# Optimization experiments

Hardware: AMD Instinct MI355X
Metric: run time of the kernel (lower is better)

The kernel has to match this reference:

```python
import jax, jax.numpy as jnp
import numpy as np

NUM_NODES = 16384   # batch_size * nodes_per_query_graph
NODES_PER_GRAPH = 8
NUM_EDGES = 14336   # ~7 edges per query graph
NUM_RELS = 64
DIM = 128
BATCH = NUM_NODES // NODES_PER_GRAPH  # 2048
NUM_PASSES = 2
EPS = 1e-8


def setup_inputs() -> dict:
    key = jax.random.key(0)
    ks = jax.random.split(key, 7)
    x = jax.random.normal(ks[0], (NUM_NODES, DIM), jnp.float32)
    basis = jax.random.normal(ks[1], (NUM_RELS, DIM, DIM), jnp.float32) * 0.05
    root = jax.random.normal(ks[2], (DIM, DIM), jnp.float32) * 0.05
    bias = jax.random.normal(ks[3], (DIM,), jnp.float32) * 0.05
    target_embeds = jax.random.normal(ks[4], (BATCH, DIM), jnp.float32)
    # edges stay within each query graph: pick local src/dst per graph
    graph_of_edge = jnp.repeat(jnp.arange(BATCH), NUM_EDGES // BATCH)
    local = jax.random.randint(ks[5], (2, NUM_EDGES), 0, NODES_PER_GRAPH)
    edge_index = graph_of_edge[None, :] * NODES_PER_GRAPH + local  # [2, E]
    edge_type = jax.random.randint(ks[6], (NUM_EDGES,), 0, NUM_RELS)
    batch_idx = jnp.arange(NUM_NODES) // NODES_PER_GRAPH  # node -> query graph id
    return {"x": x, "basis": basis, "root": root, "bias": bias,
            "target_embeds": target_embeds, "edge_index": edge_index,
            "edge_type": edge_type, "batch_idx": batch_idx}


def rgcn_conv(h, edge_index, edge_type, basis, root, bias):
    # RGCNConv forward (num_bases=0, 'add' aggregation, no edge_norm)
    src, dst = edge_index[0], edge_index[1]
    w = basis[edge_type]                      # [E, D, D] relation-indexed gather
    msg = jnp.einsum('ed,edo->eo', h[src], w)  # per-edge bmm
    aggr = jax.ops.segment_sum(msg, dst, num_segments=h.shape[0])  # scatter-add
    return aggr + h @ root + bias


def reference(x, basis, root, bias, target_embeds, edge_index, edge_type, batch_idx):
    h = x
    for _ in range(NUM_PASSES - 1):
        h = jax.nn.relu(rgcn_conv(h, edge_index, edge_type, basis, root, bias))
    # sum readout per query graph (dropout=0 -> h2 == h1)
    pooled = jax.ops.segment_sum(h, batch_idx, num_segments=target_embeds.shape[0])
    # F.cosine_similarity(out, target_embeds, dim=1)
    num = jnp.sum(pooled * target_embeds, axis=1)
    na = jnp.maximum(jnp.linalg.norm(pooled, axis=1), EPS)
    nb = jnp.maximum(jnp.linalg.norm(target_embeds, axis=1), EPS)
    return num / (na * nb)
```

## Files before the change

kernel.cpp:

```cpp
#include <hip/hip_runtime.h>

#define NUM_NODES 16384
#define NPG 8
#define NUM_EDGES 14336
#define EPG 7
#define NUM_RELS 64
#define DIM 128
#define BATCH 2048
#define EPS 1e-8f

#define SEG 1792
#define ROOT_BLOCKS 256
#define EDGE_BLOCKS 512

using f16x8 = __attribute__((ext_vector_type(8))) _Float16;
using f32x4 = __attribute__((ext_vector_type(4))) float;

#define MSG_OFF 0u
#define RTP_OFF 3670016u
#define WS_NEEDED 7864320u

__global__ __launch_bounds__(256) void gemm2_kernel(
    const float* __restrict__ x, const float* __restrict__ basis,
    const float* __restrict__ root, const int* __restrict__ edge_index,
    const int* __restrict__ edge_type,
    _Float16* __restrict__ msg_h, _Float16* __restrict__ rootp_h)
{
    __shared__ _Float16 Bl[DIM * DIM];
    __shared__ int smeta[128];
    __shared__ int lcnt;

    const int bid = blockIdx.x;
    const int tid = threadIdx.x;
    const int lane = tid & 63;
    const int w    = tid >> 6;
    const bool isEdge = bid >= ROOT_BLOCKS;

    const float* Bsrc;

    if (isEdge) {
        if (tid < 64) { smeta[tid] = 0; smeta[64 + tid] = -1; }
        if (tid == 0) lcnt = 0;
        Bsrc = basis + ((size_t)((bid - ROOT_BLOCKS) >> 3) << 14);
    } else {
        const int row0 = bid * 64;
        if (tid < 64) {
            smeta[tid] = row0 + tid;
            smeta[64 + tid] = row0 + tid;
        }
        Bsrc = root;
    }
    __syncthreads();

    if (isEdge) {
        const int eb   = bid - ROOT_BLOCKS;
        const int rel  = eb >> 3;
        const int seg0 = (eb & 7) * SEG;
        #pragma unroll
        for (int it = 0; it < 7; ++it) {
            const int e = seg0 + it * 256 + tid;
            if (edge_type[e] == rel) {
                const int pos = atomicAdd(&lcnt, 1);
                if (pos < 64) {
                    smeta[pos] = edge_index[e];
                    smeta[64 + pos] = e;
                }
            }
        }
    }

    {
        const int br = tid >> 4;
        const int bc = tid & 15;
        const float* src = Bsrc + (br * 8) * DIM + bc * 8;
        _Float16 m[8][8];
        #pragma unroll
        for (int u = 0; u < 8; ++u) {
            const float4 a = *(const float4*)(src + u * DIM);
            const float4 b = *(const float4*)(src + u * DIM + 4);
            m[u][0] = (_Float16)a.x; m[u][1] = (_Float16)a.y;
            m[u][2] = (_Float16)a.z; m[u][3] = (_Float16)a.w;
            m[u][4] = (_Float16)b.x; m[u][5] = (_Float16)b.y;
            m[u][6] = (_Float16)b.z; m[u][7] = (_Float16)b.w;
        }
        #pragma unroll
        for (int c2 = 0; c2 < 8; ++c2) {
            const int col = bc * 8 + c2;
            const int chunk = col * 16 + br;
            const int cs = chunk ^ (c2 & 7) ^ (bc & 7);
            f16x8 v = {m[0][c2], m[1][c2], m[2][c2], m[3][c2],
                       m[4][c2], m[5][c2], m[6][c2], m[7][c2]};
            *(f16x8*)(&Bl[cs * 8]) = v;
        }
    }
    __syncthreads();

    if (isEdge && lcnt == 0) return;

    const int l15 = lane & 15;
    const int q   = lane >> 4;

    const int src = smeta[w * 16 + l15];
    const float* xrow = x + ((size_t)src << 7) + q * 8;
    f16x8 a[4];
    #pragma unroll
    for (int kb = 0; kb < 4; ++kb) {
        const float4 lo = *(const float4*)(xrow + kb * 32);
        const float4 hi = *(const float4*)(xrow + kb * 32 + 4);
        f16x8 av;
        av[0] = (_Float16)lo.x; av[1] = (_Float16)lo.y;
        av[2] = (_Float16)lo.z; av[3] = (_Float16)lo.w;
        av[4] = (_Float16)hi.x; av[5] = (_Float16)hi.y;
        av[6] = (_Float16)hi.z; av[7] = (_Float16)hi.w;
        a[kb] = av;
    }

    f32x4 acc[8];
    #pragma unroll
    for (int ct = 0; ct < 8; ++ct) acc[ct] = (f32x4){0.f, 0.f, 0.f, 0.f};

    #pragma unroll
    for (int ct = 0; ct < 8; ++ct) {
        const int col = ct * 16 + l15;
        const int sw  = (col & 7) ^ ((col >> 3) & 7);
        #pragma unroll
        for (int kb = 0; kb < 4; ++kb) {
            const int chunk = col * 16 + kb * 4 + q;
            const int cs = chunk ^ sw;
            const f16x8 bfr = *(const f16x8*)(&Bl[cs * 8]);
            acc[ct] = __builtin_amdgcn_mfma_f32_16x16x32_f16(a[kb], bfr, acc[ct], 0, 0, 0);
        }
    }

    _Float16* outb = isEdge ? msg_h : rootp_h;
    #pragma unroll
    for (int j = 0; j < 4; ++j) {
        const int r = w * 16 + q * 4 + j;
        const int oid = smeta[64 + r];
        if (oid >= 0) {
            #pragma unroll
            for (int ct = 0; ct < 8; ++ct) {
                outb[((size_t)oid << 7) + ct * 16 + l15] = (_Float16)acc[ct][j];
            }
        }
    }
}

__global__ __launch_bounds__(512) void finalize_kernel(
    const _Float16* __restrict__ rootp_h, const _Float16* __restrict__ msg_h,
    const float* __restrict__ bias, const float* __restrict__ target,
    const int* __restrict__ edge_index, float* __restrict__ out)
{
    const int g = blockIdx.x * 8 + (threadIdx.x >> 6);
    const int l = threadIdx.x & 63;
    const int d0 = l * 2;

    const float2 bv = *(const float2*)(bias + d0);
    float accA[NPG], accB[NPG];
    #pragma unroll
    for (int n = 0; n < NPG; ++n) {
        const _Float16* row = rootp_h + ((size_t)(g * NPG + n) << 7) + d0;
        accA[n] = bv.x + (float)row[0];
        accB[n] = bv.y + (float)row[1];
    }

    const int ebase = g * EPG;
    #pragma unroll
    for (int e = 0; e < EPG; ++e) {
        const int ge  = ebase + e;
        const int dst = edge_index[NUM_EDGES + ge] - g * NPG;
        const _Float16* mrow = msg_h + ((size_t)ge << 7) + d0;
        const float m0 = (float)mrow[0];
        const float m1 = (float)mrow[1];
        #pragma unroll
        for (int n = 0; n < NPG; ++n) {
            accA[n] += (n == dst) ? m0 : 0.f;
            accB[n] += (n == dst) ? m1 : 0.f;
        }
    }

    float p0 = 0.f, p1 = 0.f;
    #pragma unroll
    for (int n = 0; n < NPG; ++n) {
        p0 += fmaxf(accA[n], 0.f);
        p1 += fmaxf(accB[n], 0.f);
    }

    const float2 tv = *(const float2*)(target + (size_t)g * DIM + d0);
    float num_p = p0 * tv.x + p1 * tv.y;
    float na_p  = p0 * p0 + p1 * p1;
    float nb_p  = tv.x * tv.x + tv.y * tv.y;

    #pragma unroll
    for (int off = 32; off > 0; off >>= 1) {
        num_p += __shfl_down(num_p, off);
        na_p  += __shfl_down(na_p, off);
        nb_p  += __shfl_down(nb_p, off);
    }
    if (l == 0) {
        const float na = fmaxf(sqrtf(na_p), EPS);
        const float nb = fmaxf(sqrtf(nb_p), EPS);
        out[g] = num_p / (na * nb);
    }
}

__global__ __launch_bounds__(128) void rgcn_fused_kernel(
    const float* __restrict__ x, const float* __restrict__ basis,
    const float* __restrict__ root, const float* __restrict__ bias,
    const float* __restrict__ target, const int* __restrict__ edge_index,
    const int* __restrict__ edge_type, float* __restrict__ out)
{
    const int g = blockIdx.x;
    const int o = threadIdx.x;
    __shared__ float xs[NPG][DIM];
    __shared__ float red[6];
    {
        const float4* xg = reinterpret_cast<const float4*>(x + (size_t)g * NPG * DIM);
        float4* xs4 = reinterpret_cast<float4*>(&xs[0][0]);
        xs4[o] = xg[o];
        xs4[o + 128] = xg[o + 128];
    }
    __syncthreads();
    float acc[NPG];
    const float b = bias[o];
    #pragma unroll
    for (int n = 0; n < NPG; ++n) acc[n] = b;
    for (int d4 = 0; d4 < DIM / 4; ++d4) {
        const float r0 = root[(d4 * 4 + 0) * DIM + o];
        const float r1 = root[(d4 * 4 + 1) * DIM + o];
        const float r2 = root[(d4 * 4 + 2) * DIM + o];
        const float r3 = root[(d4 * 4 + 3) * DIM + o];
        #pragma unroll
        for (int n = 0; n < NPG; ++n) {
            const float4 xv = reinterpret_cast<const float4*>(&xs[n][0])[d4];
            acc[n] += xv.x * r0 + xv.y * r1 + xv.z * r2 + xv.w * r3;
        }
    }
    const int ebase = g * EPG;
    for (int e = 0; e < EPG; ++e) {
        const int ge  = ebase + e;
        const int src = edge_index[ge] - g * NPG;
        const int dst = edge_index[NUM_EDGES + ge] - g * NPG;
        const int rel = edge_type[ge];
        const float* __restrict__ B = basis + (size_t)rel * DIM * DIM;
        float m = 0.f;
        for (int d4 = 0; d4 < DIM / 4; ++d4) {
            const float4 xv = reinterpret_cast<const float4*>(&xs[src][0])[d4];
            m += xv.x * B[(d4 * 4 + 0) * DIM + o];
            m += xv.y * B[(d4 * 4 + 1) * DIM + o];
            m += xv.z * B[(d4 * 4 + 2) * DIM + o];
            m += xv.w * B[(d4 * 4 + 3) * DIM + o];
        }
        #pragma unroll
        for (int n = 0; n < NPG; ++n) acc[n] += (n == dst) ? m : 0.f;
    }
    float p = 0.f;
    #pragma unroll
    for (int n = 0; n < NPG; ++n) p += fmaxf(acc[n], 0.f);
    const float t = target[(size_t)g * DIM + o];
    float num_p = p * t, na_p = p * p, nb_p = t * t;
    #pragma unroll
    for (int off = 32; off > 0; off >>= 1) {
        num_p += __shfl_down(num_p, off);
        na_p  += __shfl_down(na_p, off);
        nb_p  += __shfl_down(nb_p, off);
    }
    const int wave = o >> 6, lane = o & 63;
    if (lane == 0) {
        red[wave * 3 + 0] = num_p;
        red[wave * 3 + 1] = na_p;
        red[wave * 3 + 2] = nb_p;
    }
    __syncthreads();
    if (o == 0) {
        const float num = red[0] + red[3];
        const float na  = fmaxf(sqrtf(red[1] + red[4]), EPS);
        const float nb  = fmaxf(sqrtf(red[2] + red[5]), EPS);
        out[g] = num / (na * nb);
    }
}

extern "C" void kernel_launch(void* const* d_in, const int* in_sizes, int n_in,
                              void* d_out, int out_size, void* d_ws, size_t ws_size,
                              hipStream_t stream) {
    const float* x          = (const float*)d_in[0];
    const float* basis      = (const float*)d_in[1];
    const float* root       = (const float*)d_in[2];
    const float* bias       = (const float*)d_in[3];
    const float* target     = (const float*)d_in[4];
    const int*   edge_index = (const int*)d_in[5];
    const int*   edge_type  = (const int*)d_in[6];
    float* out = (float*)d_out;

    if (ws_size < WS_NEEDED) {
        rgcn_fused_kernel<<<BATCH, 128, 0, stream>>>(
            x, basis, root, bias, target, edge_index, edge_type, out);
        return;
    }

    char* ws = (char*)d_ws;
    _Float16* msg_h   = (_Float16*)(ws + MSG_OFF);
    _Float16* rootp_h = (_Float16*)(ws + RTP_OFF);

    gemm2_kernel<<<ROOT_BLOCKS + EDGE_BLOCKS, 256, 0, stream>>>(
        x, basis, root, edge_index, edge_type, msg_h, rootp_h);
    finalize_kernel<<<BATCH / 8, 512, 0, stream>>>(
        rootp_h, msg_h, bias, target, edge_index, out);
}
```

Baseline: 22.25 us.

## Fuse finalize into GEMM kernel using per-edge ready flags and spin-waits

Merges the two launches into one kernel. Edge blocks are reordered to run first, and each publishes per-edge READY flags after a release fence. Root blocks keep their root-projection tile in LDS, spin on the flags for their 56 edges, then do the per-graph aggregation, ReLU, pooling and cosine similarity in place. This removes a kernel launch and the global round trip of the root projection. In exchange it relies on edge blocks being scheduled before or alongside the root blocks, and spin-waiting risks stalls or deadlock if they are not.

```diff
diff --git a/kernel.cpp b/kernel.cpp
--- a/kernel.cpp
+++ b/kernel.cpp
@@ -10,21 +10,25 @@
 #define EPS 1e-8f
 
 #define SEG 1792
+#define EDGE_BLOCKS 512
 #define ROOT_BLOCKS 256
-#define EDGE_BLOCKS 512
-
+#define READY 0x5A5A5A5A
+
+using f16x2 = __attribute__((ext_vector_type(2))) _Float16;
 using f16x8 = __attribute__((ext_vector_type(8))) _Float16;
 using f32x4 = __attribute__((ext_vector_type(4))) float;
 
-#define MSG_OFF 0u
-#define RTP_OFF 3670016u
-#define WS_NEEDED 7864320u
-
-__global__ __launch_bounds__(256) void gemm2_kernel(
+#define FLG_OFF 0u
+#define MSG_OFF 57344u
+#define DUM_OFF 3727360u
+#define WS_NEEDED 3727616u
+
+__global__ __launch_bounds__(256, 4) void rgcn_one_kernel(
     const float* __restrict__ x, const float* __restrict__ basis,
-    const float* __restrict__ root, const int* __restrict__ edge_index,
-    const int* __restrict__ edge_type,
-    _Float16* __restrict__ msg_h, _Float16* __restrict__ rootp_h)
+    const float* __restrict__ root, const float* __restrict__ bias,
+    const float* __restrict__ target, const int* __restrict__ edge_index,
+    const int* __restrict__ edge_type, float* __restrict__ out,
+    int* __restrict__ flags, _Float16* __restrict__ msg_h, int* __restrict__ dummy)
 {
     __shared__ _Float16 Bl[DIM * DIM];
     __shared__ int smeta[128];
@@ -34,16 +38,16 @@
     const int tid = threadIdx.x;
     const int lane = tid & 63;
     const int w    = tid >> 6;
-    const bool isEdge = bid >= ROOT_BLOCKS;
+    const bool isEdge = bid < EDGE_BLOCKS;
 
     const float* Bsrc;
 
     if (isEdge) {
         if (tid < 64) { smeta[tid] = 0; smeta[64 + tid] = -1; }
         if (tid == 0) lcnt = 0;
-        Bsrc = basis + ((size_t)((bid - ROOT_BLOCKS) >> 3) << 14);
+        Bsrc = basis + ((size_t)(bid >> 3) << 14);
     } else {
-        const int row0 = bid * 64;
+        const int row0 = (bid - EDGE_BLOCKS) * 64;
         if (tid < 64) {
             smeta[tid] = row0 + tid;
             smeta[64 + tid] = row0 + tid;
@@ -53,9 +57,8 @@
     __syncthreads();
 
     if (isEdge) {
-        const int eb   = bid - ROOT_BLOCKS;
-        const int rel  = eb >> 3;
-        const int seg0 = (eb & 7) * SEG;
+        const int rel  = bid >> 3;
+        const int seg0 = (bid & 7) * SEG;
         #pragma unroll
         for (int it = 0; it < 7; ++it) {
             const int e = seg0 + it * 256 + tid;
@@ -85,8 +88,7 @@
         }
         #pragma unroll
         for (int c2 = 0; c2 < 8; ++c2) {
-            const int col = bc * 8 + c2;
-            const int chunk = col * 16 + br;
+            const int chunk = (bc * 8 + c2) * 16 + br;
             const int cs = chunk ^ (c2 & 7) ^ (bc & 7);
             f16x8 v = {m[0][c2], m[1][c2], m[2][c2], m[3][c2],
                        m[4][c2], m[5][c2], m[6][c2], m[7][c2]};
@@ -100,8 +102,8 @@
     const int l15 = lane & 15;
     const int q   = lane >> 4;
 
-    const int src = smeta[w * 16 + l15];
-    const float* xrow = x + ((size_t)src << 7) + q * 8;
+    const int srcn = smeta[w * 16 + l15];
+    const float* xrow = x + ((size_t)srcn << 7) + q * 8;
     f16x8 a[4];
     #pragma unroll
     for (int kb = 0; kb < 4; ++kb) {
@@ -126,81 +128,111 @@
         #pragma unroll
         for (int kb = 0; kb < 4; ++kb) {
             const int chunk = col * 16 + kb * 4 + q;
-            const int cs = chunk ^ sw;
-            const f16x8 bfr = *(const f16x8*)(&Bl[cs * 8]);
+            const f16x8 bfr = *(const f16x8*)(&Bl[(chunk ^ sw) * 8]);
             acc[ct] = __builtin_amdgcn_mfma_f32_16x16x32_f16(a[kb], bfr, acc[ct], 0, 0, 0);
         }
     }
 
-    _Float16* outb = isEdge ? msg_h : rootp_h;
+    if (isEdge) {
+        #pragma unroll
+        for (int j = 0; j < 4; ++j) {
+            const int r = w * 16 + q * 4 + j;
+            const int oid = smeta[64 + r];
+            if (oid >= 0) {
+                #pragma unroll
+                for (int ct = 0; ct < 8; ++ct)
+                    msg_h[((size_t)oid << 7) + ct * 16 + l15] = (_Float16)acc[ct][j];
+            }
+        }
+        __syncthreads();
+        if (tid == 0)
+            __hip_atomic_fetch_add(dummy, 1, __ATOMIC_RELEASE, __HIP_MEMORY_SCOPE_AGENT);
+        __syncthreads();
+        if (tid < 64) {
+            const int oid = smeta[64 + tid];
+            if (oid >= 0)
+                (void)__hip_atomic_exchange(flags + oid, READY,
+                                            __ATOMIC_RELAXED, __HIP_MEMORY_SCOPE_AGENT);
+        }
+        return;
+    }
+
+    __syncthreads();
+    _Float16* Cl = Bl;
     #pragma unroll
     for (int j = 0; j < 4; ++j) {
-        const int r = w * 16 + q * 4 + j;
-        const int oid = smeta[64 + r];
-        if (oid >= 0) {
+        const int lr = w * 16 + q * 4 + j;
+        #pragma unroll
+        for (int ct = 0; ct < 8; ++ct)
+            Cl[lr * 132 + ct * 16 + l15] = (_Float16)acc[ct][j];
+    }
+    __syncthreads();
+
+    const int rb = bid - EDGE_BLOCKS;
+    if (w == 0 && lane < 56) {
+        int* fp = flags + rb * 56 + lane;
+        while (__hip_atomic_load(fp, __ATOMIC_RELAXED, __HIP_MEMORY_SCOPE_AGENT) != READY)
+            __builtin_amdgcn_s_sleep(2);
+        __hip_atomic_store(fp, 0, __ATOMIC_RELAXED, __HIP_MEMORY_SCOPE_AGENT);
+    }
+    __syncthreads();
+    if (tid == 0)
+        (void)__hip_atomic_load(dummy, __ATOMIC_ACQUIRE, __HIP_MEMORY_SCOPE_AGENT);
+    __syncthreads();
+
+    #pragma unroll
+    for (int k = 0; k < 2; ++k) {
+        const int lg = w * 2 + k;
+        const int g  = rb * 8 + lg;
+        const int d0 = lane * 2;
+
+        const float2 bv = *(const float2*)(bias + d0);
+        float accA[NPG], accB[NPG];
+        #pragma unroll
+        for (int n = 0; n < NPG; ++n) {
+            const f16x2 c = *(const f16x2*)(&Cl[(lg * 8 + n) * 132 + d0]);
+            accA[n] = bv.x + (float)c[0];
+            accB[n] = bv.y + (float)c[1];
+        }
+
+        const int ebase = g * EPG;
+        #pragma unroll
+        for (int e = 0; e < EPG; ++e) {
+            const int ge  = ebase + e;
+            const int dst = edge_index[NUM_EDGES + ge] - g * NPG;
+            const f16x2 mv = *(const f16x2*)(msg_h + ((size_t)ge << 7) + d0);
+            const float m0 = (float)mv[0];
+            const float m1 = (float)mv[1];
             #pragma unroll
-            for (int ct = 0; ct < 8; ++ct) {
-                outb[((size_t)oid << 7) + ct * 16 + l15] = (_Float16)acc[ct][j];
+            for (int n = 0; n < NPG; ++n) {
+                accA[n] += (n == dst) ? m0 : 0.f;
+                accB[n] += (n == dst) ? m1 : 0.f;
             }
         }
-    }
-}
-
-__global__ __launch_bounds__(512) void finalize_kernel(
-    const _Float16* __restrict__ rootp_h, const _Float16* __restrict__ msg_h,
-    const float* __restrict__ bias, const float* __restrict__ target,
-    const int* __restrict__ edge_index, float* __restrict__ out)
-{
-    const int g = blockIdx.x * 8 + (threadIdx.x >> 6);
-    const int l = threadIdx.x & 63;
-    const int d0 = l * 2;
-
-    const float2 bv = *(const float2*)(bias + d0);
-    float accA[NPG], accB[NPG];
-    #pragma unroll
-    for (int n = 0; n < NPG; ++n) {
-        const _Float16* row = rootp_h + ((size_t)(g * NPG + n) << 7) + d0;
-        accA[n] = bv.x + (float)row[0];
-        accB[n] = bv.y + (float)row[1];
-    }
-
-    const int ebase = g * EPG;
-    #pragma unroll
-    for (int e = 0; e < EPG; ++e) {
-        const int ge  = ebase + e;
-        const int dst = edge_index[NUM_EDGES + ge] - g * NPG;
-        const _Float16* mrow = msg_h + ((size_t)ge << 7) + d0;
-        const float m0 = (float)mrow[0];
-        const float m1 = (float)mrow[1];
+
+        float p0 = 0.f, p1 = 0.f;
         #pragma unroll
         for (int n = 0; n < NPG; ++n) {
-            accA[n] += (n == dst) ? m0 : 0.f;
-            accB[n] += (n == dst) ? m1 : 0.f;
-        }
-    }
-
-    float p0 = 0.f, p1 = 0.f;
-    #pragma unroll
-    for (int n = 0; n < NPG; ++n) {
-        p0 += fmaxf(accA[n], 0.f);
-        p1 += fmaxf(accB[n], 0.f);
-    }
-
-    const float2 tv = *(const float2*)(target + (size_t)g * DIM + d0);
-    float num_p = p0 * tv.x + p1 * tv.y;
-    float na_p  = p0 * p0 + p1 * p1;
-    float nb_p  = tv.x * tv.x + tv.y * tv.y;
-
-    #pragma unroll
-    for (int off = 32; off > 0; off >>= 1) {
-        num_p += __shfl_down(num_p, off);
-        na_p  += __shfl_down(na_p, off);
-        nb_p  += __shfl_down(nb_p, off);
-    }
-    if (l == 0) {
-        const float na = fmaxf(sqrtf(na_p), EPS);
-        const float nb = fmaxf(sqrtf(nb_p), EPS);
-        out[g] = num_p / (na * nb);
+            p0 += fmaxf(accA[n], 0.f);
+            p1 += fmaxf(accB[n], 0.f);
+        }
+
+        const float2 tv = *(const float2*)(target + (size_t)g * DIM + d0);
+        float num_p = p0 * tv.x + p1 * tv.y;
+        float na_p  = p0 * p0 + p1 * p1;
+        float nb_p  = tv.x * tv.x + tv.y * tv.y;
+
+        #pragma unroll
+        for (int off = 32; off > 0; off >>= 1) {
+            num_p += __shfl_down(num_p, off);
+            na_p  += __shfl_down(na_p, off);
+            nb_p  += __shfl_down(nb_p, off);
+        }
+        if (lane == 0) {
+            const float na = fmaxf(sqrtf(na_p), EPS);
+            const float nb = fmaxf(sqrtf(nb_p), EPS);
+            out[g] = num_p / (na * nb);
+        }
     }
 }
 
@@ -299,11 +331,11 @@
     }
 
     char* ws = (char*)d_ws;
-    _Float16* msg_h   = (_Float16*)(ws + MSG_OFF);
-    _Float16* rootp_h = (_Float16*)(ws + RTP_OFF);
-
-    gemm2_kernel<<<ROOT_BLOCKS + EDGE_BLOCKS, 256, 0, stream>>>(
-        x, basis, root, edge_index, edge_type, msg_h, rootp_h);
-    finalize_kernel<<<BATCH / 8, 512, 0, stream>>>(
-        rootp_h, msg_h, bias, target, edge_index, out);
+    int*      flags = (int*)(ws + FLG_OFF);
+    _Float16* msg_h = (_Float16*)(ws + MSG_OFF);
+    int*      dummy = (int*)(ws + DUM_OFF);
+
+    rgcn_one_kernel<<<EDGE_BLOCKS + ROOT_BLOCKS, 256, 0, stream>>>(
+        x, basis, root, bias, target, edge_index, edge_type, out,
+        flags, msg_h, dummy);
 }
```

After: 38.89 us. 1.75x slower.

## Process multiple 64-row strips per block to amortize weight staging

Applied to the files above, without the earlier changes.

Blocks now handle up to 256 root rows or 128 edges per relation, looping over 64-row strips. Each block therefore converts and stages a 128x128 weight matrix into shared memory for more rows, and the grid shrinks from 768 to 320 blocks. This cuts redundant basis and root loads and conversions, at the cost of less parallelism and a longer serial loop per block.

```diff
diff --git a/kernel.cpp b/kernel.cpp
--- a/kernel.cpp
+++ b/kernel.cpp
@@ -9,10 +9,11 @@
 #define BATCH 2048
 #define EPS 1e-8f
 
-#define SEG 1792
-#define ROOT_BLOCKS 256
-#define EDGE_BLOCKS 512
-
+#define SEG 3584
+#define ROOT_BLOCKS 64
+#define EDGE_BLOCKS 256
+
+using f16x2 = __attribute__((ext_vector_type(2))) _Float16;
 using f16x8 = __attribute__((ext_vector_type(8))) _Float16;
 using f32x4 = __attribute__((ext_vector_type(4))) float;
 
@@ -20,14 +21,15 @@
 #define RTP_OFF 3670016u
 #define WS_NEEDED 7864320u
 
-__global__ __launch_bounds__(256) void gemm2_kernel(
+__global__ __launch_bounds__(256, 4) void gemm2_kernel(
     const float* __restrict__ x, const float* __restrict__ basis,
     const float* __restrict__ root, const int* __restrict__ edge_index,
     const int* __restrict__ edge_type,
     _Float16* __restrict__ msg_h, _Float16* __restrict__ rootp_h)
 {
     __shared__ _Float16 Bl[DIM * DIM];
-    __shared__ int smeta[128];
+    __shared__ int ssrc[128];
+    __shared__ int soid[128];
     __shared__ int lcnt;
 
     const int bid = blockIdx.x;
@@ -37,33 +39,27 @@
     const bool isEdge = bid >= ROOT_BLOCKS;
 
     const float* Bsrc;
-
     if (isEdge) {
-        if (tid < 64) { smeta[tid] = 0; smeta[64 + tid] = -1; }
+        if (tid < 128) { ssrc[tid] = 0; soid[tid] = -1; }
         if (tid == 0) lcnt = 0;
-        Bsrc = basis + ((size_t)((bid - ROOT_BLOCKS) >> 3) << 14);
+        Bsrc = basis + ((size_t)((bid - ROOT_BLOCKS) >> 2) << 14);
     } else {
-        const int row0 = bid * 64;
-        if (tid < 64) {
-            smeta[tid] = row0 + tid;
-            smeta[64 + tid] = row0 + tid;
-        }
         Bsrc = root;
     }
     __syncthreads();
 
     if (isEdge) {
         const int eb   = bid - ROOT_BLOCKS;
-        const int rel  = eb >> 3;
-        const int seg0 = (eb & 7) * SEG;
-        #pragma unroll
-        for (int it = 0; it < 7; ++it) {
+        const int rel  = eb >> 2;
+        const int seg0 = (eb & 3) * SEG;
+        #pragma unroll
+        for (int it = 0; it < 14; ++it) {
             const int e = seg0 + it * 256 + tid;
             if (edge_type[e] == rel) {
                 const int pos = atomicAdd(&lcnt, 1);
-                if (pos < 64) {
-                    smeta[pos] = edge_index[e];
-                    smeta[64 + pos] = e;
+                if (pos < 128) {
+                    ssrc[pos] = edge_index[e];
+                    soid[pos] = e;
                 }
             }
         }
@@ -85,8 +81,7 @@
         }
         #pragma unroll
         for (int c2 = 0; c2 < 8; ++c2) {
-            const int col = bc * 8 + c2;
-            const int chunk = col * 16 + br;
+            const int chunk = (bc * 8 + c2) * 16 + br;
             const int cs = chunk ^ (c2 & 7) ^ (bc & 7);
             f16x8 v = {m[0][c2], m[1][c2], m[2][c2], m[3][c2],
                        m[4][c2], m[5][c2], m[6][c2], m[7][c2]};
@@ -95,52 +90,61 @@
     }
     __syncthreads();
 
-    if (isEdge && lcnt == 0) return;
+    int nstrips;
+    const int row0 = bid * 256;
+    if (isEdge) {
+        const int nr = min(lcnt, 128);
+        if (nr == 0) return;
+        nstrips = (nr + 63) >> 6;
+    } else {
+        nstrips = 4;
+    }
 
     const int l15 = lane & 15;
     const int q   = lane >> 4;
-
-    const int src = smeta[w * 16 + l15];
-    const float* xrow = x + ((size_t)src << 7) + q * 8;
-    f16x8 a[4];
-    #pragma unroll
-    for (int kb = 0; kb < 4; ++kb) {
-        const float4 lo = *(const float4*)(xrow + kb * 32);
-        const float4 hi = *(const float4*)(xrow + kb * 32 + 4);
-        f16x8 av;
-        av[0] = (_Float16)lo.x; av[1] = (_Float16)lo.y;
-        av[2] = (_Float16)lo.z; av[3] = (_Float16)lo.w;
-        av[4] = (_Float16)hi.x; av[5] = (_Float16)hi.y;
-        av[6] = (_Float16)hi.z; av[7] = (_Float16)hi.w;
-        a[kb] = av;
-    }
-
-    f32x4 acc[8];
-    #pragma unroll
-    for (int ct = 0; ct < 8; ++ct) acc[ct] = (f32x4){0.f, 0.f, 0.f, 0.f};
-
-    #pragma unroll
-    for (int ct = 0; ct < 8; ++ct) {
-        const int col = ct * 16 + l15;
-        const int sw  = (col & 7) ^ ((col >> 3) & 7);
+    _Float16* outb = isEdge ? msg_h : rootp_h;
+
+    for (int s = 0; s < nstrips; ++s) {
+        const int ridx = s * 64 + w * 16 + l15;
+        const int srcn = isEdge ? ssrc[ridx] : (row0 + ridx);
+        const float* xrow = x + ((size_t)srcn << 7) + q * 8;
+        f16x8 a[4];
         #pragma unroll
         for (int kb = 0; kb < 4; ++kb) {
-            const int chunk = col * 16 + kb * 4 + q;
-            const int cs = chunk ^ sw;
-            const f16x8 bfr = *(const f16x8*)(&Bl[cs * 8]);
-            acc[ct] = __builtin_amdgcn_mfma_f32_16x16x32_f16(a[kb], bfr, acc[ct], 0, 0, 0);
-        }
-    }
-
-    _Float16* outb = isEdge ? msg_h : rootp_h;
-    #pragma unroll
-    for (int j = 0; j < 4; ++j) {
-        const int r = w * 16 + q * 4 + j;
-        const int oid = smeta[64 + r];
-        if (oid >= 0) {
+            const float4 lo = *(const float4*)(xrow + kb * 32);
+            const float4 hi = *(const float4*)(xrow + kb * 32 + 4);
+            f16x8 av;
+            av[0] = (_Float16)lo.x; av[1] = (_Float16)lo.y;
+            av[2] = (_Float16)lo.z; av[3] = (_Float16)lo.w;
+            av[4] = (_Float16)hi.x; av[5] = (_Float16)hi.y;
+            av[6] = (_Float16)hi.z; av[7] = (_Float16)hi.w;
+            a[kb] = av;
+        }
+
+        f32x4 acc[8];
+        #pragma unroll
+        for (int ct = 0; ct < 8; ++ct) acc[ct] = (f32x4){0.f, 0.f, 0.f, 0.f};
+
+        #pragma unroll
+        for (int ct = 0; ct < 8; ++ct) {
+            const int col = ct * 16 + l15;
+            const int sw  = (col & 7) ^ ((col >> 3) & 7);
             #pragma unroll
-            for (int ct = 0; ct < 8; ++ct) {
-                outb[((size_t)oid << 7) + ct * 16 + l15] = (_Float16)acc[ct][j];
+            for (int kb = 0; kb < 4; ++kb) {
+                const int chunk = col * 16 + kb * 4 + q;
+                const f16x8 bfr = *(const f16x8*)(&Bl[(chunk ^ sw) * 8]);
+                acc[ct] = __builtin_amdgcn_mfma_f32_16x16x32_f16(a[kb], bfr, acc[ct], 0, 0, 0);
+            }
+        }
+
+        #pragma unroll
+        for (int j = 0; j < 4; ++j) {
+            const int r = s * 64 + w * 16 + q * 4 + j;
+            const int oid = isEdge ? soid[r] : (row0 + r);
+            if (oid >= 0) {
+                #pragma unroll
+                for (int ct = 0; ct < 8; ++ct)
+                    outb[((size_t)oid << 7) + ct * 16 + l15] = (_Float16)acc[ct][j];
             }
         }
     }
```

Measured after the change: 37.69 us. 69.4% more time.
